# Optimization experiments

Measured on AMD Instinct MI355X. Metric: run time of the kernel, lower is better.

Reference implementation:

```python
import jax, jax.numpy as jnp
import numpy as np

B, T, C, N = 4, 12, 64, 10000
H = 64            # d_inner (GRU hidden)
L = 2             # num_layers
NE = 2000         # number of static hyperedges
NNZ = 80000       # incidence list length
TOPK = 10         # HGCNADP_topk
DE = 16           # HGCNADP_embed_dims
RATE = 0.5        # hyperedge_rate (blend static vs adaptive)


def setup_inputs() -> dict:
    key = jax.random.key(0)
    ks = jax.random.split(key, 10)
    scale = 0.05
    x = jax.random.normal(ks[0], (B, T, C, N), jnp.float32)
    node_idx = jax.random.randint(ks[1], (NNZ,), 0, N, jnp.int32)
    edge_idx = jax.random.randint(ks[2], (NNZ,), 0, NE, jnp.int32)
    hyperedge_index = jnp.stack([node_idx, edge_idx])  # (2, NNZ)
    node_embs = jax.random.normal(ks[3], (L, N, DE), jnp.float32) * 0.1
    W_zr = jax.random.normal(ks[4], (L, C + H, 2 * H), jnp.float32) * scale
    b_zr = jnp.zeros((L, 2 * H), jnp.float32)
    W_c = jax.random.normal(ks[5], (L, C + H, H), jnp.float32) * scale
    b_c = jnp.zeros((L, H), jnp.float32)
    W_out = jax.random.normal(ks[6], (L, H, C), jnp.float32) * scale
    b_out = jnp.zeros((L, C), jnp.float32)
    return {"x": x, "hyperedge_index": hyperedge_index, "node_embs": node_embs,
            "W_zr": W_zr, "b_zr": b_zr, "W_c": W_c, "b_c": b_c,
            "W_out": W_out, "b_out": b_out}


def reference(x, hyperedge_index, node_embs, W_zr, b_zr, W_c, b_c, W_out, b_out):
    # x: (B, T, C, N). Dropout is identity (eval mode).
    node_idx = hyperedge_index[0]
    edge_idx = hyperedge_index[1]
    edge_deg = jnp.zeros((NE,), x.dtype).at[edge_idx].add(1.0)
    inv_e = 1.0 / jnp.maximum(edge_deg, 1.0)
    node_deg = jnp.zeros((N,), x.dtype).at[node_idx].add(1.0)
    inv_n = 1.0 / jnp.maximum(node_deg, 1.0)

    def conv(f, topk_idx, topk_w):
        # f: (B, N, D). Static hypergraph pass: node -> hyperedge -> node.
        msg = jnp.take(f, node_idx, axis=1)                       # (B, NNZ, D)
        eagg = jnp.zeros((f.shape[0], NE, f.shape[2]), f.dtype).at[:, edge_idx].add(msg)
        eagg = eagg * inv_e[None, :, None]                        # (B, NE, D)
        stat = jnp.zeros_like(f).at[:, node_idx].add(jnp.take(eagg, edge_idx, axis=1))
        stat = stat * inv_n[None, :, None]                        # (B, N, D)
        # Adaptive top-k hyperedge aggregation (softmax-weighted neighbor sum).
        adp = jnp.einsum('bnkd,nk->bnd', jnp.take(f, topk_idx, axis=1), topk_w)
        return RATE * stat + (1.0 - RATE) * adp

    out = x
    for l in range(L):
        xl = out.transpose(0, 1, 3, 2)                            # (B, T, N, C)
        E = node_embs[l]
        scores = jax.nn.relu(E @ E.T)                             # (N, N)
        vals, idx = jax.lax.top_k(scores, TOPK)                   # (N, K)
        w = jax.nn.softmax(vals, axis=-1)
        Wz, bz = W_zr[l], b_zr[l]
        Wc_, bc_ = W_c[l], b_c[l]
        Wo, bo = W_out[l], b_out[l]

        def step(h, x_t):
            zr = jax.nn.sigmoid(conv(jnp.concatenate([x_t, h], -1), idx, w) @ Wz + bz)
            z, r = jnp.split(zr, 2, axis=-1)
            c = jnp.tanh(conv(jnp.concatenate([x_t, r * h], -1), idx, w) @ Wc_ + bc_)
            h_new = z * h + (1.0 - z) * c
            return h_new, h_new @ Wo + bo

        h0 = jnp.zeros((out.shape[0], N, H), x.dtype)
        _, ys = jax.lax.scan(step, h0, xl.transpose(1, 0, 2, 3))  # ys: (T, B, N, C)
        out = out + ys.transpose(1, 0, 3, 2)                      # residual, back to (B,T,C,N)
    return out
```

## Files before the change

kernel.cpp:

```cpp
#include <hip/hip_runtime.h>
#include <hip/hip_fp16.h>
#include <cstdio>

#define BB 4
#define TT 12
#define CC 64
#define NN 10000
#define HH 64
#define LL 2
#define NEDGE 2000
#define NNZT 80000
#define KTOP 10
#define DEMB 16
#define BT (BB*TT)
#define TOPK_BLKS 1250
#define TRN_BLKS 30048

typedef long long ll;
typedef unsigned long long u64;
typedef unsigned int u32;
typedef unsigned short ushort;

typedef short bf16x8 __attribute__((ext_vector_type(8)));
typedef float f32x4 __attribute__((ext_vector_type(4)));

__device__ __forceinline__ void up8(const uint4 v, float* f) {
  const __half2* p = reinterpret_cast<const __half2*>(&v);
  float2 t0 = __half22float2(p[0]);
  float2 t1 = __half22float2(p[1]);
  float2 t2 = __half22float2(p[2]);
  float2 t3 = __half22float2(p[3]);
  f[0]=t0.x; f[1]=t0.y; f[2]=t1.x; f[3]=t1.y;
  f[4]=t2.x; f[5]=t2.y; f[6]=t3.x; f[7]=t3.y;
}
__device__ __forceinline__ uint4 pk8(const float* f) {
  __half2 h0 = __floats2half2_rn(f[0], f[1]);
  __half2 h1 = __floats2half2_rn(f[2], f[3]);
  __half2 h2 = __floats2half2_rn(f[4], f[5]);
  __half2 h3 = __floats2half2_rn(f[6], f[7]);
  uint4 r;
  r.x = *reinterpret_cast<unsigned*>(&h0);
  r.y = *reinterpret_cast<unsigned*>(&h1);
  r.z = *reinterpret_cast<unsigned*>(&h2);
  r.w = *reinterpret_cast<unsigned*>(&h3);
  return r;
}
__device__ __forceinline__ ushort f2bf(float x) {
  u32 u = __float_as_uint(x);
  u32 r = u + 0x7FFFu + ((u >> 16) & 1u);
  return (ushort)(r >> 16);
}
__device__ __forceinline__ uint4 pk8bf(const float* f) {
  uint4 r;
  r.x = (u32)f2bf(f[0]) | ((u32)f2bf(f[1])<<16);
  r.y = (u32)f2bf(f[2]) | ((u32)f2bf(f[3])<<16);
  r.z = (u32)f2bf(f[4]) | ((u32)f2bf(f[5])<<16);
  r.w = (u32)f2bf(f[6]) | ((u32)f2bf(f[7])<<16);
  return r;
}

__global__ void deg_kernel(const int* __restrict__ nidx, const int* __restrict__ eidx,
                           int* __restrict__ ndeg, int* __restrict__ edeg) {
  int i = blockIdx.x*256 + threadIdx.x;
  if (i < NNZT) { atomicAdd(&ndeg[nidx[i]],1); atomicAdd(&edeg[eidx[i]],1); }
}

__global__ void exscan_kernel(const int* __restrict__ cnt, int* __restrict__ off, int n) {
  __shared__ int part[256];
  int tid = threadIdx.x;
  int chunk = (n + 255)/256;
  int lo = tid*chunk, hi = min(lo+chunk, n);
  int s = 0;
  for (int i=lo; i<hi; ++i) s += cnt[i];
  part[tid]=s; __syncthreads();
  if (tid==0){ int acc=0; for(int i=0;i<256;++i){int v=part[i];part[i]=acc;acc+=v;} off[n]=acc; }
  __syncthreads();
  int acc = part[tid];
  for (int i=lo; i<hi; ++i){ off[i]=acc; acc+=cnt[i]; }
}

__global__ void fill_csr_kernel(const int* __restrict__ nidx, const int* __restrict__ eidx,
                                const int* __restrict__ noff, const int* __restrict__ eoff,
                                int* __restrict__ ncur, int* __restrict__ ecur,
                                int* __restrict__ node_edges, int* __restrict__ edge_nodes) {
  int i = blockIdx.x*256 + threadIdx.x;
  if (i >= NNZT) return;
  int n = nidx[i], e = eidx[i];
  int pn = atomicAdd(&ncur[n],1);
  node_edges[noff[n]+pn] = e;
  int pe = atomicAdd(&ecur[e],1);
  edge_nodes[eoff[e]+pe] = n;
}

__global__ void invdeg_kernel(const int* __restrict__ ndeg, const int* __restrict__ edeg,
                              float* __restrict__ inv_n, float* __restrict__ inv_e) {
  int i = blockIdx.x*256+threadIdx.x;
  if (i < NN) inv_n[i] = 1.0f/fmaxf((float)ndeg[i],1.0f);
  if (i < NEDGE) inv_e[i] = 1.0f/fmaxf((float)edeg[i],1.0f);
}

__global__ void prep_w_kernel(const float* __restrict__ W_zr, const float* __restrict__ W_c,
                              const float* __restrict__ W_o,
                              short* __restrict__ Wz_swb, short* __restrict__ Wc_swb,
                              short* __restrict__ Wo_swb) {
  int l = blockIdx.y;
  const float* Wz = W_zr + (size_t)l*128*128;
  const float* Wc = W_c  + (size_t)l*128*64;
  const float* Wo = W_o  + (size_t)l*64*64;
  short* Wz_sw = Wz_swb + (size_t)l*16384;
  short* Wc_sw = Wc_swb + (size_t)l*8192;
  short* Wo_sw = Wo_swb + (size_t)l*4096;
  int idx = blockIdx.x*256 + threadIdx.x;
  if (idx < 16384) {
    int i = idx&7, lane = (idx>>3)&63, kk = (idx>>9)&3, tc = idx>>11;
    int k = kk*32 + (lane>>4)*8 + i, col = tc*16 + (lane&15);
    Wz_sw[idx] = (short)f2bf(Wz[k*128+col]);
  }
  if (idx < 8192) {
    int i = idx&7, lane = (idx>>3)&63, kk = (idx>>9)&3, tc = idx>>11;
    int k = kk*32 + (lane>>4)*8 + i, col = tc*16 + (lane&15);
    Wc_sw[idx] = (short)f2bf(Wc[k*64+col]);
  }
  if (idx < 4096) {
    int i = idx&7, lane = (idx>>3)&63, kk = (idx>>9)&1, tc = idx>>10;
    int k = kk*32 + (lane>>4)*8 + i, col = tc*16 + (lane&15);
    Wo_sw[idx] = (short)f2bf(Wo[k*64+col]);
  }
}

__device__ __forceinline__ u64 sortstep(u64 X, int j, bool dir, int lane) {
  u64 p = __shfl_xor(X, j);
  bool lower = ((lane & j) == 0);
  bool keep_min = (dir == lower);
  bool xlt = (X < p);
  u64 mn = xlt ? X : p;
  u64 mx = xlt ? p : X;
  return keep_min ? mn : mx;
}

__device__ __forceinline__ void reselect(u64* bq, u64& thr, int& cnt, int lane) {
  int tot = 10 + cnt;
  u64 A = (lane < tot)      ? bq[lane]      : 0ull;
  u64 B = (lane + 64 < tot) ? bq[lane + 64] : 0ull;
  for (int k = 2; k <= 32; k <<= 1) {
    for (int j = k >> 1; j >= 1; j >>= 1) {
      bool dir = ((lane & k) == 0);
      A = sortstep(A, j, dir, lane);
      B = sortstep(B, j, dir, lane);
    }
  }
  for (int j = 32; j >= 1; j >>= 1) {
    A = sortstep(A, j, true,  lane);
    B = sortstep(B, j, false, lane);
  }
  {
    bool lt = (A < B);
    u64 mn = lt ? A : B, mx = lt ? B : A;
    A = mn; B = mx;
  }
  for (int j = 32; j >= 1; j >>= 1) {
    A = sortstep(A, j, true, lane);
    B = sortstep(B, j, true, lane);
  }
  if (lane >= 54) bq[63 - lane] = B;
  thr = __shfl(B, 54);
  cnt = 0;
}

__device__ void topk_body(int layer, int qb, char* smem,
                          const float* __restrict__ embs, int2* __restrict__ tkc_b) {
  u64 (*buf)[128] = (u64(*)[128])smem;
  const float* E = embs + (ll)layer*NN*DEMB;
  int2* tkc = tkc_b + (ll)layer*NN*KTOP;
  int tid = threadIdx.x;
  int wv = tid >> 6, lane = tid & 63;
  int qbase = qb*16 + wv*4;
  const float4* E4 = (const float4*)E;
  float4 q[4][4];
  #pragma unroll
  for (int u=0;u<4;++u) {
    int n = qbase + u;
    #pragma unroll
    for (int j=0;j<4;++j) q[u][j] = E4[(ll)n*4 + j];
  }
  u64 thr[4] = {0,0,0,0};
  float thrf[4] = {0.f,0.f,0.f,0.f};
  int cnt[4] = {0,0,0,0};
  buf[tid>>4][tid&15] = 0ull;
  for (int cb=0; cb<NN; cb+=64) {
    int cand = cb + lane;
    bool valid = (cand < NN);
    int ca = valid ? cand : 0;
    float4 a0 = E4[(ll)ca*4], a1 = E4[(ll)ca*4+1], a2 = E4[(ll)ca*4+2], a3 = E4[(ll)ca*4+3];
    u64 low = (u64)(0x00FFFFFFu - (unsigned)cand);
    float sv[4];
    #pragma unroll
    for (int u=0;u<4;++u) {
      float dot = q[u][0].x*a0.x + q[u][0].y*a0.y + q[u][0].z*a0.z + q[u][0].w*a0.w
                + q[u][1].x*a1.x + q[u][1].y*a1.y + q[u][1].z*a1.z + q[u][1].w*a1.w
                + q[u][2].x*a2.x + q[u][2].y*a2.y + q[u][2].z*a2.z + q[u][2].w*a2.w
                + q[u][3].x*a3.x + q[u][3].y*a3.y + q[u][3].z*a3.z + q[u][3].w*a3.w;
      float s = fmaxf(dot, 0.f);
      sv[u] = valid ? s : -1.f;
    }
    #pragma unroll
    for (int u=0;u<4;++u) {
      u64 mask = __ballot(sv[u] >= thrf[u]);
      if (mask) {
        if (sv[u] >= thrf[u]) {
          u64 key = ((u64)__float_as_uint(sv[u]) << 32) | low;
          int myofs = (int)__popcll(mask & ((1ull<<lane)-1ull));
          buf[wv*4+u][10 + cnt[u] + myofs] = key;
        }
        cnt[u] += (int)__popcll(mask);
        if (cnt[u] >= 40) {
          reselect(&buf[wv*4+u][0], thr[u], cnt[u], lane);
          thrf[u] = __uint_as_float((u32)(thr[u] >> 32));
        }
      }
    }
  }
  #pragma unroll
  for (int u=0;u<4;++u) {
    u64* bq = &buf[wv*4+u][0];
    if (cnt[u] > 0) reselect(bq, thr[u], cnt[u], lane);
    u64 k10 = (lane < 10) ? bq[lane] : 0ull;
    float v = __uint_as_float((unsigned)(k10 >> 32));
    int idx = 0x00FFFFFF - (int)(k10 & 0xFFFFFFFFull);
    float v0 = __shfl(v, 0);
    float e = (lane < 10) ? expf(v - v0) : 0.f;
    float s = e;
    for (int o=1;o<16;o<<=1) s += __shfl_xor(s, o);
    if (lane < 10) {
      int n = qbase + u;
      tkc[n*KTOP + lane] = make_int2(idx, __float_as_int(e / s));
    }
  }
}

__device__ void transpose_body(int tb, char* smem,
                               const float* __restrict__ src, __half* __restrict__ dst) {
  float (*tile)[33] = (float(*)[33])smem;
  int tid = threadIdx.x;
  int tx = tid & 31, ty = tid >> 5;
  int bt = tb / 626;
  int rem = tb % 626;
  int n0 = (rem % 313)*32, c0 = (rem/313)*32;
  for (int i=ty; i<32; i+=8) {
    int c = c0+i, nn = n0+tx;
    tile[i][tx] = (nn<NN)? src[((ll)bt*CC + c)*NN + nn] : 0.0f;
  }
  __syncthreads();
  for (int i=ty; i<32; i+=8) {
    int nn = n0+i, c = c0+tx;
    if (nn<NN) dst[((ll)bt*NN+nn)*64 + c] = __float2half_rn(tile[tx][i]);
  }
}

__global__ void __launch_bounds__(256) mega1_kernel(const float* __restrict__ embs,
                                                    int2* __restrict__ tkc,
                                                    const float* __restrict__ x,
                                                    __half* __restrict__ xt) {
  __shared__ __align__(16) char smem[16384];
  int bid = blockIdx.x;
  if (bid < TOPK_BLKS) topk_body(bid/625, bid%625, smem, embs, tkc);
  else transpose_body(bid - TOPK_BLKS, smem, x, xt);
}

__global__ void transpose_kernel(const float* __restrict__ src, __half* __restrict__ dst) {
  __shared__ __align__(16) char smem[4352];
  int tb = (blockIdx.z*626) + blockIdx.y*313 + blockIdx.x;
  transpose_body(tb, smem, src, dst);
}

__global__ void __launch_bounds__(256) edge_agg_kernel(
    const uint4* __restrict__ f8, uint4* __restrict__ eagg8,
    const int* __restrict__ eoff, const int* __restrict__ enodes,
    const float* __restrict__ inv_e) {
  __shared__ int en_s[1088];
  __shared__ int jo_s[17];
  int tid = threadIdx.x;
  int e0 = blockIdx.x*16;
  int s = blockIdx.y;
  if (tid < 17) jo_s[tid] = eoff[e0 + tid];
  __syncthreads();
  int jb0 = jo_s[0], cnt = jo_s[16] - jb0;
  bool stg = (cnt <= 1088);
  if (stg) for (int i = tid; i < cnt; i += 256) en_s[i] = enodes[jb0 + i];
  __syncthreads();
  int esub = tid>>4;
  int e = e0 + esub;
  int hsel = (tid>>3)&1;
  int lane8 = tid&7;
  int j0 = jo_s[esub] - jb0, j1 = jo_s[esub+1] - jb0;
  const uint4* fb = f8 + (ll)s*NN*8;
  float acc[8] = {0,0,0,0,0,0,0,0};
  for (int j = j0 + hsel; j < j1; j += 2) {
    int node = stg ? en_s[j] : enodes[jb0+j];
    float t[8]; up8(fb[(ll)node*8 + lane8], t);
    #pragma unroll
    for (int q=0;q<8;++q) acc[q] += t[q];
  }
  #pragma unroll
  for (int q=0;q<8;++q) acc[q] += __shfl_xor(acc[q], 8);
  if (hsel == 0) {
    float sc = inv_e[e];
    #pragma unroll
    for (int q=0;q<8;++q) acc[q] *= sc;
    eagg8[((ll)s*NEDGE+e)*8 + lane8] = pk8(acc);
  }
}

__global__ void __launch_bounds__(256) conv_x_kernel(
    const uint4* __restrict__ xt8, const uint4* __restrict__ eagg8,
    const int* __restrict__ noff, const int* __restrict__ nedges,
    const float* __restrict__ inv_n,
    const int2* __restrict__ tkc,
    uint4* __restrict__ cx8) {
  __shared__ int tki_s[32][KTOP];
  __shared__ float tkw_s[32][KTOP];
  __shared__ int ne_s[640];
  __shared__ int no_s[33];
  int tid = threadIdx.x; int s = blockIdx.y; int n0 = blockIdx.x*32;
  if (tid < 33) no_s[tid] = noff[min(n0 + tid, NN)];
  for (int i=tid; i<32*KTOP; i+=256) {
    int r=i/KTOP, k=i%KTOP; int n = n0+r;
    int2 p = (n<NN)? tkc[n*KTOP+k] : make_int2(0,0);
    tki_s[r][k] = p.x;
    tkw_s[r][k] = __int_as_float(p.y);
  }
  __syncthreads();
  int jb0 = no_s[0], cnt = no_s[32] - jb0;
  bool stg = (cnt <= 640);
  if (stg) for (int i=tid; i<cnt; i+=256) ne_s[i] = nedges[jb0+i];
  __syncthreads();
  int row = tid>>3, lane8 = tid&7;
  int n = n0 + row;
  if (n >= NN) return;
  float stv[8] = {0,0,0,0,0,0,0,0};
  const uint4* eb = eagg8 + (ll)s*NEDGE*8;
  int j0 = no_s[row] - jb0, j1 = no_s[row+1] - jb0;
  for (int j=j0;j<j1;++j) {
    int eidx = stg ? ne_s[j] : nedges[jb0+j];
    float t[8]; up8(eb[(ll)eidx*8 + lane8], t);
    #pragma unroll
    for (int q=0;q<8;++q) stv[q] += t[q];
  }
  float sc = 0.5f*inv_n[n];
  float adv[8] = {0,0,0,0,0,0,0,0};
  const uint4* xb = xt8 + (ll)s*NN*8;
  #pragma unroll
  for (int k=0;k<KTOP;++k) {
    float w = tkw_s[row][k];
    float t[8]; up8(xb[(ll)tki_s[row][k]*8 + lane8], t);
    #pragma unroll
    for (int q=0;q<8;++q) adv[q] += w*t[q];
  }
  float r8[8];
  #pragma unroll
  for (int q=0;q<8;++q) r8[q] = sc*stv[q] + 0.5f*adv[q];
  cx8[((ll)s*NN+n)*8+lane8] = pk8bf(r8);
}

__global__ void __launch_bounds__(256) step0_kernel(
    const uint4* __restrict__ cx8,
    const short* __restrict__ Wz_sw, const float* __restrict__ bz,
    const short* __restrict__ Wc_sw, const float* __restrict__ bc,
    const short* __restrict__ Wo_sw, const float* __restrict__ bo,
    __half* __restrict__ h, float* __restrict__ out) {
  __shared__ __align__(16) short in_bf[32][72];
  __shared__ __align__(16) short hn[32][72];
  __shared__ __align__(16) float yt[64][36];
  int tid = threadIdx.x;
  int b = blockIdx.y; int n0 = blockIdx.x*32;
  int bt = b*TT;
  {
    int row = tid>>3, lane8 = tid&7;
    int n = n0 + row;
    uint4 cxv4 = make_uint4(0,0,0,0);
    if (n < NN) cxv4 = cx8[((ll)bt*NN + n)*8 + lane8];
    *(uint4*)&in_bf[row][lane8*8] = cxv4;
  }
  __syncthreads();
  int wv = tid>>6, lane = tid&63;
  int m = lane&15, g = lane>>4;
  #pragma unroll
  for (int q=0;q<2;++q) {
    int T = wv + 4*q;
    int tr = T>>2, tc = T&3;
    f32x4 az = {0.f,0.f,0.f,0.f};
    f32x4 ac = {0.f,0.f,0.f,0.f};
    #pragma unroll
    for (int kk=0;kk<2;++kk) {
      bf16x8 a = *(const bf16x8*)&in_bf[tr*16 + m][kk*32 + g*8];
      bf16x8 bwz = *(const bf16x8*)&Wz_sw[((tc*4+kk)*64 + lane)*8];
      bf16x8 bwc = *(const bf16x8*)&Wc_sw[((tc*4+kk)*64 + lane)*8];
      az = __builtin_amdgcn_mfma_f32_16x16x32_bf16(a, bwz, az, 0, 0, 0);
      ac = __builtin_amdgcn_mfma_f32_16x16x32_bf16(a, bwc, ac, 0, 0, 0);
    }
    int col = tc*16 + m;
    float bzv = bz[col], bcv = bc[col];
    #pragma unroll
    for (int r=0;r<4;++r) {
      int row = tr*16 + g*4 + r;
      int n = n0 + row;
      float z = 1.0f/(1.0f+expf(-(az[r]+bzv)));
      float cval = tanhf(ac[r]+bcv);
      float hnew = (1.0f-z)*cval;
      if (n < NN) h[((ll)b*NN+n)*64+col] = __float2half_rn(hnew);
      hn[row][col] = (short)f2bf(hnew);
    }
  }
  __syncthreads();
  #pragma unroll
  for (int q=0;q<2;++q) {
    int T = wv + 4*q;
    int tr = T>>2, tc = T&3;
    f32x4 acc = {0.f,0.f,0.f,0.f};
    #pragma unroll
    for (int kk=0;kk<2;++kk) {
      bf16x8 a = *(const bf16x8*)&hn[tr*16 + m][kk*32 + g*8];
      bf16x8 bw = *(const bf16x8*)&Wo_sw[((tc*2+kk)*64 + lane)*8];
      acc = __builtin_amdgcn_mfma_f32_16x16x32_bf16(a, bw, acc, 0, 0, 0);
    }
    int col = tc*16 + m;
    float bias = bo[col];
    #pragma unroll
    for (int r=0;r<4;++r) {
      int row = tr*16 + g*4 + r;
      yt[col][row] = acc[r] + bias;
    }
  }
  __syncthreads();
  #pragma unroll
  for (int kk=0;kk<2;++kk) {
    int slot = tid + kk*256;
    int col = slot>>3, q = slot&7;
    int n = n0 + q*4;
    if (n < NN) {
      float4 y = *(const float4*)&yt[col][q*4];
      float4* dst = (float4*)&out[((ll)bt*64+col)*NN + n];
      float4 cur = *dst;
      cur.x += y.x; cur.y += y.y; cur.z += y.z; cur.w += y.w;
      *dst = cur;
    }
  }
}

__global__ void __launch_bounds__(256) step_zr_kernel(
    const uint4* __restrict__ h8, const uint4* __restrict__ cx8,
    const uint4* __restrict__ eagg8,
    const short* __restrict__ Wz_sw, const float* __restrict__ bz,
    const int* __restrict__ noff, const int* __restrict__ nedges,
    const float* __restrict__ inv_n,
    const int2* __restrict__ tkc,
    const __half* __restrict__ hs,
    __half* __restrict__ rh, __half* __restrict__ zout, int t) {
  __shared__ __align__(16) short in_bf[32][136];
  __shared__ int tki_s[32][KTOP];
  __shared__ float tkw_s[32][KTOP];
  __shared__ int ne_s[640];
  __shared__ int no_s[33];
  int tid = threadIdx.x;
  int b = blockIdx.y; int n0 = blockIdx.x*32;
  int bt = b*TT + t;
  if (tid < 33) no_s[tid] = noff[min(n0 + tid, NN)];
  for (int i=tid; i<32*KTOP; i+=256) {
    int r=i/KTOP, k=i%KTOP; int n=n0+r;
    int2 p = (n<NN)? tkc[n*KTOP+k] : make_int2(0,0);
    tki_s[r][k] = p.x;
    tkw_s[r][k] = __int_as_float(p.y);
  }
  __syncthreads();
  int jb0 = no_s[0], ecnt = no_s[32] - jb0;
  bool stg = (ecnt <= 640);
  if (stg) for (int i=tid; i<ecnt; i+=256) ne_s[i] = nedges[jb0+i];
  __syncthreads();
  {
    int row = tid>>3, lane8 = tid&7;
    int n = n0 + row;
    uint4 cxv4 = make_uint4(0,0,0,0);
    float chv[8] = {0,0,0,0,0,0,0,0};
    if (n < NN) {
      cxv4 = cx8[((ll)bt*NN + n)*8 + lane8];
      float stv[8] = {0,0,0,0,0,0,0,0};
      int j0 = no_s[row] - jb0, j1 = no_s[row+1] - jb0;
      const uint4* eb = eagg8 + (ll)b*NEDGE*8;
      for (int j=j0;j<j1;++j) {
        int eidx = stg ? ne_s[j] : nedges[jb0+j];
        float t8[8]; up8(eb[(ll)eidx*8 + lane8], t8);
        #pragma unroll
        for (int q=0;q<8;++q) stv[q] += t8[q];
      }
      float sc = 0.5f*inv_n[n];
      const uint4* hb = h8 + (ll)b*NN*8;
      float adv[8] = {0,0,0,0,0,0,0,0};
      #pragma unroll
      for (int k=0;k<KTOP;++k) {
        float w = tkw_s[row][k];
        float t8[8]; up8(hb[(ll)tki_s[row][k]*8 + lane8], t8);
        #pragma unroll
        for (int q=0;q<8;++q) adv[q] += w*t8[q];
      }
      #pragma unroll
      for (int q=0;q<8;++q) chv[q] = sc*stv[q] + 0.5f*adv[q];
    }
    *(uint4*)&in_bf[row][lane8*8]    = cxv4;
    *(uint4*)&in_bf[row][64+lane8*8] = pk8bf(chv);
  }
  __syncthreads();
  int wv = tid>>6, lane = tid&63;
  int m = lane&15, g = lane>>4;
  #pragma unroll
  for (int q=0;q<4;++q) {
    int T = wv*4 + q;
    int tr = T>>3, tc = T&7;
    f32x4 acc = {0.f,0.f,0.f,0.f};
    #pragma unroll
    for (int kk=0;kk<4;++kk) {
      bf16x8 a = *(const bf16x8*)&in_bf[tr*16 + m][kk*32 + g*8];
      bf16x8 bf = *(const bf16x8*)&Wz_sw[((tc*4+kk)*64 + lane)*8];
      acc = __builtin_amdgcn_mfma_f32_16x16x32_bf16(a, bf, acc, 0, 0, 0);
    }
    int col = tc*16 + m;
    float bias = bz[col];
    #pragma unroll
    for (int r=0;r<4;++r) {
      int row = tr*16 + g*4 + r;
      int n = n0 + row;
      if (n < NN) {
        float v = 1.0f/(1.0f+expf(-(acc[r]+bias)));
        if (col < 64) zout[((ll)b*NN+n)*64+col] = __float2half_rn(v);
        else {
          int c = col-64;
          float hv = __half2float(hs[((ll)b*NN+n)*64+c]);
          rh[((ll)b*NN+n)*64+c] = __float2half_rn(v*hv);
        }
      }
    }
  }
}

__global__ void __launch_bounds__(256) step_hy_kernel(
    const uint4* __restrict__ rh8, const uint4* __restrict__ cx8,
    const uint4* __restrict__ eagg8,
    const short* __restrict__ Wc_sw, const float* __restrict__ bc,
    const short* __restrict__ Wo_sw, const float* __restrict__ bo,
    const int* __restrict__ noff, const int* __restrict__ nedges,
    const float* __restrict__ inv_n,
    const int2* __restrict__ tkc,
    const __half* __restrict__ zbuf, __half* __restrict__ h,
    float* __restrict__ out, int t) {
  __shared__ __align__(16) short in_bf[32][136];
  __shared__ __align__(16) short hn[32][72];
  __shared__ __align__(16) float yt[64][36];
  __shared__ int tki_s[32][KTOP];
  __shared__ float tkw_s[32][KTOP];
  __shared__ int ne_s[640];
  __shared__ int no_s[33];
  int tid = threadIdx.x;
  int b = blockIdx.y; int n0 = blockIdx.x*32;
  int bt = b*TT + t;
  if (tid < 33) no_s[tid] = noff[min(n0 + tid, NN)];
  for (int i=tid; i<32*KTOP; i+=256) {
    int r=i/KTOP, k=i%KTOP; int n=n0+r;
    int2 p = (n<NN)? tkc[n*KTOP+k] : make_int2(0,0);
    tki_s[r][k] = p.x;
    tkw_s[r][k] = __int_as_float(p.y);
  }
  __syncthreads();
  int jb0 = no_s[0], ecnt = no_s[32] - jb0;
  bool stg = (ecnt <= 640);
  if (stg) for (int i=tid; i<ecnt; i+=256) ne_s[i] = nedges[jb0+i];
  __syncthreads();
  {
    int row = tid>>3, lane8 = tid&7;
    int n = n0 + row;
    uint4 cxv4 = make_uint4(0,0,0,0);
    float chv[8] = {0,0,0,0,0,0,0,0};
    if (n < NN) {
      cxv4 = cx8[((ll)bt*NN + n)*8 + lane8];
      float stv[8] = {0,0,0,0,0,0,0,0};
      int j0 = no_s[row] - jb0, j1 = no_s[row+1] - jb0;
      const uint4* eb = eagg8 + (ll)b*NEDGE*8;
      for (int j=j0;j<j1;++j) {
        int eidx = stg ? ne_s[j] : nedges[jb0+j];
        float t8[8]; up8(eb[(ll)eidx*8 + lane8], t8);
        #pragma unroll
        for (int q=0;q<8;++q) stv[q] += t8[q];
      }
      float sc = 0.5f*inv_n[n];
      const uint4* rb = rh8 + (ll)b*NN*8;
      float adv[8] = {0,0,0,0,0,0,0,0};
      #pragma unroll
      for (int k=0;k<KTOP;++k) {
        float w = tkw_s[row][k];
        float t8[8]; up8(rb[(ll)tki_s[row][k]*8 + lane8], t8);
        #pragma unroll
        for (int q=0;q<8;++q) adv[q] += w*t8[q];
      }
      #pragma unroll
      for (int q=0;q<8;++q) chv[q] = sc*stv[q] + 0.5f*adv[q];
    }
    *(uint4*)&in_bf[row][lane8*8]    = cxv4;
    *(uint4*)&in_bf[row][64+lane8*8] = pk8bf(chv);
  }
  __syncthreads();
  int wv = tid>>6, lane = tid&63;
  int m = lane&15, g = lane>>4;
  #pragma unroll
  for (int q=0;q<2;++q) {
    int T = wv + 4*q;
    int tr = T>>2, tc = T&3;
    f32x4 acc = {0.f,0.f,0.f,0.f};
    #pragma unroll
    for (int kk=0;kk<4;++kk) {
      bf16x8 a = *(const bf16x8*)&in_bf[tr*16 + m][kk*32 + g*8];
      bf16x8 bf = *(const bf16x8*)&Wc_sw[((tc*4+kk)*64 + lane)*8];
      acc = __builtin_amdgcn_mfma_f32_16x16x32_bf16(a, bf, acc, 0, 0, 0);
    }
    int col = tc*16 + m;
    float bias = bc[col];
    #pragma unroll
    for (int r=0;r<4;++r) {
      int row = tr*16 + g*4 + r;
      int n = n0 + row;
      float hnew = 0.0f;
      if (n < NN) {
        float cval = tanhf(acc[r]+bias);
        float z = __half2float(zbuf[((ll)b*NN+n)*64+col]);
        float hv = __half2float(h[((ll)b*NN+n)*64+col]);
        hnew = z*hv + (1.0f-z)*cval;
        h[((ll)b*NN+n)*64+col] = __float2half_rn(hnew);
      }
      hn[row][col] = (short)f2bf(hnew);
    }
  }
  __syncthreads();
  #pragma unroll
  for (int q=0;q<2;++q) {
    int T = wv + 4*q;
    int tr = T>>2, tc = T&3;
    f32x4 acc = {0.f,0.f,0.f,0.f};
    #pragma unroll
    for (int kk=0;kk<2;++kk) {
      bf16x8 a = *(const bf16x8*)&hn[tr*16 + m][kk*32 + g*8];
      bf16x8 bf = *(const bf16x8*)&Wo_sw[((tc*2+kk)*64 + lane)*8];
      acc = __builtin_amdgcn_mfma_f32_16x16x32_bf16(a, bf, acc, 0, 0, 0);
    }
    int col = tc*16 + m;
    float bias = bo[col];
    #pragma unroll
    for (int r=0;r<4;++r) {
      int row = tr*16 + g*4 + r;
      yt[col][row] = acc[r] + bias;
    }
  }
  __syncthreads();
  #pragma unroll
  for (int kk=0;kk<2;++kk) {
    int slot = tid + kk*256;
    int col = slot>>3, q = slot&7;
    int n = n0 + q*4;
    if (n < NN) {
      float4 y = *(const float4*)&yt[col][q*4];
      float4* dst = (float4*)&out[((ll)bt*64+col)*NN + n];
      float4 cur = *dst;
      cur.x += y.x; cur.y += y.y; cur.z += y.z; cur.w += y.w;
      *dst = cur;
    }
  }
}

extern "C" void kernel_launch(void* const* d_in, const int* in_sizes, int n_in,
                              void* d_out, int out_size, void* d_ws, size_t ws_size,
                              hipStream_t stream) {
  const float* x    = (const float*)d_in[0];
  const int*  hidx  = (const int*)d_in[1];
  const float* embs = (const float*)d_in[2];
  const float* W_zr = (const float*)d_in[3];
  const float* b_zr = (const float*)d_in[4];
  const float* W_c  = (const float*)d_in[5];
  const float* b_c  = (const float*)d_in[6];
  const float* W_out= (const float*)d_in[7];
  const float* b_out= (const float*)d_in[8];
  const int* node_idx = hidx;
  const int* edge_idx = hidx + NNZT;

  char* ws = (char*)d_ws;
  size_t off = 0;
  auto alloc = [&](size_t bytes) -> void* {
    void* p = ws + off; off += (bytes + 255) & ~(size_t)255; return p;
  };
  __half* xt    = (__half*)alloc((size_t)BT*NN*64*2);
  __half* cx    = (__half*)alloc((size_t)BT*NN*64*2);
  __half* eaggx = (__half*)alloc((size_t)BT*NEDGE*64*2);
  __half* eaggh = (__half*)alloc((size_t)BB*NEDGE*64*2);
  __half* hbuf  = (__half*)alloc((size_t)BB*NN*64*2);
  __half* rhbuf = (__half*)alloc((size_t)BB*NN*64*2);
  __half* zbuf  = (__half*)alloc((size_t)BB*NN*64*2);
  short* Wz_sw = (short*)alloc((size_t)LL*16384*2);
  short* Wc_sw = (short*)alloc((size_t)LL*8192*2);
  short* Wo_sw = (short*)alloc((size_t)LL*4096*2);
  int2* tkc    = (int2*)alloc((size_t)LL*NN*KTOP*8);
  float* inv_e = (float*)alloc(NEDGE*4);
  float* inv_n = (float*)alloc(NN*4);
  int* ndeg    = (int*)alloc(NN*4);
  int* edeg    = (int*)alloc(NEDGE*4);
  int* noff    = (int*)alloc((NN+1)*4);
  int* eoff    = (int*)alloc((NEDGE+1)*4);
  int* ncur    = (int*)alloc(NN*4);
  int* ecur    = (int*)alloc(NEDGE*4);
  int* nedges  = (int*)alloc(NNZT*4);
  int* enodes  = (int*)alloc(NNZT*4);
  if (off > ws_size) {
    fprintf(stderr, "kernel_launch: ws too small, need %zu have %zu\n", off, ws_size);
    return;
  }

  hipMemcpyAsync(d_out, x, (size_t)BB*TT*CC*NN*4, hipMemcpyDeviceToDevice, stream);

  hipMemsetAsync(ndeg, 0, NN*4, stream);
  hipMemsetAsync(edeg, 0, NEDGE*4, stream);
  hipMemsetAsync(ncur, 0, NN*4, stream);
  hipMemsetAsync(ecur, 0, NEDGE*4, stream);
  deg_kernel<<<(NNZT+255)/256,256,0,stream>>>(node_idx, edge_idx, ndeg, edeg);
  exscan_kernel<<<1,256,0,stream>>>(ndeg, noff, NN);
  exscan_kernel<<<1,256,0,stream>>>(edeg, eoff, NEDGE);
  fill_csr_kernel<<<(NNZT+255)/256,256,0,stream>>>(node_idx, edge_idx, noff, eoff,
                                                   ncur, ecur, nedges, enodes);
  invdeg_kernel<<<(NN+255)/256,256,0,stream>>>(ndeg, edeg, inv_n, inv_e);

  prep_w_kernel<<<dim3(64,LL),256,0,stream>>>(W_zr, W_c, W_out, Wz_sw, Wc_sw, Wo_sw);
  float* outp = (float*)d_out;
  mega1_kernel<<<TOPK_BLKS + TRN_BLKS,256,0,stream>>>(embs, tkc, outp, xt);

  for (int l=0; l<LL; ++l) {
    const short* Wzs = Wz_sw + (size_t)l*16384;
    const short* Wcs = Wc_sw + (size_t)l*8192;
    const short* Wos = Wo_sw + (size_t)l*4096;
    const float* bz = b_zr + l*128;
    const float* bc = b_c + l*64;
    const float* bo = b_out + l*64;
    const int2* tkcl = tkc + (size_t)l*NN*KTOP;
    if (l > 0)
      transpose_kernel<<<dim3(313, 2, BT), 256, 0, stream>>>(outp, xt);
    edge_agg_kernel<<<dim3(125, BT),256,0,stream>>>(
        (const uint4*)xt, (uint4*)eaggx, eoff, enodes, inv_e);
    conv_x_kernel<<<dim3(313, BT),256,0,stream>>>(
        (const uint4*)xt, (const uint4*)eaggx, noff, nedges, inv_n, tkcl, (uint4*)cx);
    step0_kernel<<<dim3(313, BB),256,0,stream>>>(
        (const uint4*)cx, Wzs, bz, Wcs, bc, Wos, bo, hbuf, outp);
    for (int t=1; t<TT; ++t) {
      edge_agg_kernel<<<dim3(125, BB),256,0,stream>>>(
          (const uint4*)hbuf, (uint4*)eaggh, eoff, enodes, inv_e);
      step_zr_kernel<<<dim3(313, BB),256,0,stream>>>(
          (const uint4*)hbuf, (const uint4*)cx, (const uint4*)eaggh, Wzs, bz,
          noff, nedges, inv_n, tkcl, hbuf, rhbuf, zbuf, t);
      edge_agg_kernel<<<dim3(125, BB),256,0,stream>>>(
          (const uint4*)rhbuf, (uint4*)eaggh, eoff, enodes, inv_e);
      step_hy_kernel<<<dim3(313, BB),256,0,stream>>>(
          (const uint4*)rhbuf, (const uint4*)cx, (const uint4*)eaggh, Wcs, bc, Wos, bo,
          noff, nedges, inv_n, tkcl, zbuf, hbuf, outp, t);
    }
  }
}
```

Baseline: 2.354 ms.

## Fuse hyperedge aggregation into GRU step kernels via fixed-point atomics

Removes the separate edge_agg launches in the recurrent loop. Each step kernel now scatters its new h or r*h values into double-buffered int32 hyperedge accumulators using scaled fixed-point atomicAdd, and the next kernel reads those sums. Each kernel also zeroes the accumulator buffer it no longer needs. Separately, the top-k scan now prefetches the next candidate tile's embeddings one iteration ahead. The cost is heavy atomic traffic, int32 accumulators that are wider than the fp16 ones they replace, a fixed-point precision and overflow risk, and zeroing that depends on buffer rotation across layers.

```diff
diff --git a/kernel.cpp b/kernel.cpp
--- a/kernel.cpp
+++ b/kernel.cpp
@@ -15,6 +15,8 @@
 #define BT (BB*TT)
 #define TOPK_BLKS 1250
 #define TRN_BLKS 30048
+#define SCALE_F 67108864.0f
+#define INV_SCALE 1.4901161193847656e-8f
 
 typedef long long ll;
 typedef unsigned long long u64;
@@ -57,6 +59,14 @@
   r.z = (u32)f2bf(f[4]) | ((u32)f2bf(f[5])<<16);
   r.w = (u32)f2bf(f[6]) | ((u32)f2bf(f[7])<<16);
   return r;
+}
+
+__device__ __forceinline__ void zero_duty(int* buf, int b, int blk) {
+  const int total = NEDGE*64;
+  int base = blk*409;
+  int hi = min(base+409, total);
+  int* p = buf + (ll)b*total;
+  for (int i = base + threadIdx.x; i < hi; i += 256) p[i] = 0;
 }
 
 __global__ void deg_kernel(const int* __restrict__ nidx, const int* __restrict__ eidx,
@@ -187,11 +197,21 @@
   float thrf[4] = {0.f,0.f,0.f,0.f};
   int cnt[4] = {0,0,0,0};
   buf[tid>>4][tid&15] = 0ull;
+  float4 a0,a1,a2,a3;
+  {
+    int ca = (lane < NN) ? lane : 0;
+    a0=E4[(ll)ca*4]; a1=E4[(ll)ca*4+1]; a2=E4[(ll)ca*4+2]; a3=E4[(ll)ca*4+3];
+  }
   for (int cb=0; cb<NN; cb+=64) {
+    float4 b0,b1,b2,b3;
+    int ncb = cb + 64;
+    if (ncb < NN) {
+      int cand2 = ncb + lane;
+      int ca2 = (cand2 < NN) ? cand2 : 0;
+      b0=E4[(ll)ca2*4]; b1=E4[(ll)ca2*4+1]; b2=E4[(ll)ca2*4+2]; b3=E4[(ll)ca2*4+3];
+    }
     int cand = cb + lane;
     bool valid = (cand < NN);
-    int ca = valid ? cand : 0;
-    float4 a0 = E4[(ll)ca*4], a1 = E4[(ll)ca*4+1], a2 = E4[(ll)ca*4+2], a3 = E4[(ll)ca*4+3];
     u64 low = (u64)(0x00FFFFFFu - (unsigned)cand);
     float sv[4];
     #pragma unroll
@@ -219,6 +239,7 @@
         }
       }
     }
+    a0=b0; a1=b1; a2=b2; a3=b3;
   }
   #pragma unroll
   for (int u=0;u<4;++u) {
@@ -367,13 +388,25 @@
     const short* __restrict__ Wz_sw, const float* __restrict__ bz,
     const short* __restrict__ Wc_sw, const float* __restrict__ bc,
     const short* __restrict__ Wo_sw, const float* __restrict__ bo,
-    __half* __restrict__ h, float* __restrict__ out) {
+    const int* __restrict__ noff, const int* __restrict__ nedges,
+    const float* __restrict__ inv_e,
+    __half* __restrict__ h, float* __restrict__ out,
+    int* __restrict__ ieh_dst, int* __restrict__ zero1, int* __restrict__ zero2) {
   __shared__ __align__(16) short in_bf[32][72];
   __shared__ __align__(16) short hn[32][72];
   __shared__ __align__(16) float yt[64][36];
+  __shared__ int ne_s[640];
+  __shared__ int no_s[33];
   int tid = threadIdx.x;
   int b = blockIdx.y; int n0 = blockIdx.x*32;
   int bt = b*TT;
+  zero_duty(zero1, b, blockIdx.x);
+  zero_duty(zero2, b, blockIdx.x);
+  if (tid < 33) no_s[tid] = noff[min(n0 + tid, NN)];
+  __syncthreads();
+  int jb0 = no_s[0], ecnt = no_s[32] - jb0;
+  bool stg = (ecnt <= 640);
+  if (stg) for (int i=tid; i<ecnt; i+=256) ne_s[i] = nedges[jb0+i];
   {
     int row = tid>>3, lane8 = tid&7;
     int n = n0 + row;
@@ -407,7 +440,15 @@
       float z = 1.0f/(1.0f+expf(-(az[r]+bzv)));
       float cval = tanhf(ac[r]+bcv);
       float hnew = (1.0f-z)*cval;
-      if (n < NN) h[((ll)b*NN+n)*64+col] = __float2half_rn(hnew);
+      if (n < NN) {
+        h[((ll)b*NN+n)*64+col] = __float2half_rn(hnew);
+        int j0 = no_s[row]-jb0, j1 = no_s[row+1]-jb0;
+        for (int j=j0;j<j1;++j) {
+          int e = stg ? ne_s[j] : nedges[jb0+j];
+          atomicAdd(&ieh_dst[((ll)b*NEDGE+e)*64 + col],
+                    __float2int_rn(hnew*inv_e[e]*SCALE_F));
+        }
+      }
       hn[row][col] = (short)f2bf(hnew);
     }
   }
@@ -449,13 +490,14 @@
 
 __global__ void __launch_bounds__(256) step_zr_kernel(
     const uint4* __restrict__ h8, const uint4* __restrict__ cx8,
-    const uint4* __restrict__ eagg8,
+    const int* __restrict__ ieh_cur,
     const short* __restrict__ Wz_sw, const float* __restrict__ bz,
     const int* __restrict__ noff, const int* __restrict__ nedges,
-    const float* __restrict__ inv_n,
+    const float* __restrict__ inv_n, const float* __restrict__ inv_e,
     const int2* __restrict__ tkc,
     const __half* __restrict__ hs,
-    __half* __restrict__ rh, __half* __restrict__ zout, int t) {
+    __half* __restrict__ rh, __half* __restrict__ zout,
+    int* __restrict__ ierh_dst, int* __restrict__ ierh_zero, int t) {
   __shared__ __align__(16) short in_bf[32][136];
   __shared__ int tki_s[32][KTOP];
   __shared__ float tkw_s[32][KTOP];
@@ -464,6 +506,7 @@
   int tid = threadIdx.x;
   int b = blockIdx.y; int n0 = blockIdx.x*32;
   int bt = b*TT + t;
+  zero_duty(ierh_zero, b, blockIdx.x);
   if (tid < 33) no_s[tid] = noff[min(n0 + tid, NN)];
   for (int i=tid; i<32*KTOP; i+=256) {
     int r=i/KTOP, k=i%KTOP; int n=n0+r;
@@ -485,14 +528,15 @@
       cxv4 = cx8[((ll)bt*NN + n)*8 + lane8];
       float stv[8] = {0,0,0,0,0,0,0,0};
       int j0 = no_s[row] - jb0, j1 = no_s[row+1] - jb0;
-      const uint4* eb = eagg8 + (ll)b*NEDGE*8;
+      const int4* ebi = (const int4*)ieh_cur + (ll)b*NEDGE*16;
       for (int j=j0;j<j1;++j) {
         int eidx = stg ? ne_s[j] : nedges[jb0+j];
-        float t8[8]; up8(eb[(ll)eidx*8 + lane8], t8);
-        #pragma unroll
-        for (int q=0;q<8;++q) stv[q] += t8[q];
+        int4 v0 = ebi[(ll)eidx*16 + lane8*2];
+        int4 v1 = ebi[(ll)eidx*16 + lane8*2 + 1];
+        stv[0]+=(float)v0.x; stv[1]+=(float)v0.y; stv[2]+=(float)v0.z; stv[3]+=(float)v0.w;
+        stv[4]+=(float)v1.x; stv[5]+=(float)v1.y; stv[6]+=(float)v1.z; stv[7]+=(float)v1.w;
       }
-      float sc = 0.5f*inv_n[n];
+      float sc = 0.5f*inv_n[n]*INV_SCALE;
       const uint4* hb = h8 + (ll)b*NN*8;
       float adv[8] = {0,0,0,0,0,0,0,0};
       #pragma unroll
@@ -534,7 +578,14 @@
         else {
           int c = col-64;
           float hv = __half2float(hs[((ll)b*NN+n)*64+c]);
-          rh[((ll)b*NN+n)*64+c] = __float2half_rn(v*hv);
+          float rhv = v*hv;
+          rh[((ll)b*NN+n)*64+c] = __float2half_rn(rhv);
+          int j0 = no_s[row]-jb0, j1 = no_s[row+1]-jb0;
+          for (int j=j0;j<j1;++j) {
+            int e = stg ? ne_s[j] : nedges[jb0+j];
+            atomicAdd(&ierh_dst[((ll)b*NEDGE+e)*64 + c],
+                      __float2int_rn(rhv*inv_e[e]*SCALE_F));
+          }
         }
       }
     }
@@ -543,14 +594,15 @@
 
 __global__ void __launch_bounds__(256) step_hy_kernel(
     const uint4* __restrict__ rh8, const uint4* __restrict__ cx8,
-    const uint4* __restrict__ eagg8,
+    const int* __restrict__ ierh_cur,
     const short* __restrict__ Wc_sw, const float* __restrict__ bc,
     const short* __restrict__ Wo_sw, const float* __restrict__ bo,
     const int* __restrict__ noff, const int* __restrict__ nedges,
-    const float* __restrict__ inv_n,
+    const float* __restrict__ inv_n, const float* __restrict__ inv_e,
     const int2* __restrict__ tkc,
     const __half* __restrict__ zbuf, __half* __restrict__ h,
-    float* __restrict__ out, int t) {
+    float* __restrict__ out,
+    int* __restrict__ ieh_dst, int* __restrict__ ieh_zero, int t) {
   __shared__ __align__(16) short in_bf[32][136];
   __shared__ __align__(16) short hn[32][72];
   __shared__ __align__(16) float yt[64][36];
@@ -561,6 +613,7 @@
   int tid = threadIdx.x;
   int b = blockIdx.y; int n0 = blockIdx.x*32;
   int bt = b*TT + t;
+  zero_duty(ieh_zero, b, blockIdx.x);
   if (tid < 33) no_s[tid] = noff[min(n0 + tid, NN)];
   for (int i=tid; i<32*KTOP; i+=256) {
     int r=i/KTOP, k=i%KTOP; int n=n0+r;
@@ -582,14 +635,15 @@
       cxv4 = cx8[((ll)bt*NN + n)*8 + lane8];
       float stv[8] = {0,0,0,0,0,0,0,0};
       int j0 = no_s[row] - jb0, j1 = no_s[row+1] - jb0;
-      const uint4* eb = eagg8 + (ll)b*NEDGE*8;
+      const int4* ebi = (const int4*)ierh_cur + (ll)b*NEDGE*16;
       for (int j=j0;j<j1;++j) {
         int eidx = stg ? ne_s[j] : nedges[jb0+j];
-        float t8[8]; up8(eb[(ll)eidx*8 + lane8], t8);
-        #pragma unroll
-        for (int q=0;q<8;++q) stv[q] += t8[q];
+        int4 v0 = ebi[(ll)eidx*16 + lane8*2];
+        int4 v1 = ebi[(ll)eidx*16 + lane8*2 + 1];
+        stv[0]+=(float)v0.x; stv[1]+=(float)v0.y; stv[2]+=(float)v0.z; stv[3]+=(float)v0.w;
+        stv[4]+=(float)v1.x; stv[5]+=(float)v1.y; stv[6]+=(float)v1.z; stv[7]+=(float)v1.w;
       }
-      float sc = 0.5f*inv_n[n];
+      float sc = 0.5f*inv_n[n]*INV_SCALE;
       const uint4* rb = rh8 + (ll)b*NN*8;
       float adv[8] = {0,0,0,0,0,0,0,0};
       #pragma unroll
@@ -632,6 +686,12 @@
         float hv = __half2float(h[((ll)b*NN+n)*64+col]);
         hnew = z*hv + (1.0f-z)*cval;
         h[((ll)b*NN+n)*64+col] = __float2half_rn(hnew);
+        int j0 = no_s[row]-jb0, j1 = no_s[row+1]-jb0;
+        for (int j=j0;j<j1;++j) {
+          int e = stg ? ne_s[j] : nedges[jb0+j];
+          atomicAdd(&ieh_dst[((ll)b*NEDGE+e)*64 + col],
+                    __float2int_rn(hnew*inv_e[e]*SCALE_F));
+        }
       }
       hn[row][col] = (short)f2bf(hnew);
     }
@@ -695,10 +755,13 @@
   __half* xt    = (__half*)alloc((size_t)BT*NN*64*2);
   __half* cx    = (__half*)alloc((size_t)BT*NN*64*2);
   __half* eaggx = (__half*)alloc((size_t)BT*NEDGE*64*2);
-  __half* eaggh = (__half*)alloc((size_t)BB*NEDGE*64*2);
   __half* hbuf  = (__half*)alloc((size_t)BB*NN*64*2);
   __half* rhbuf = (__half*)alloc((size_t)BB*NN*64*2);
   __half* zbuf  = (__half*)alloc((size_t)BB*NN*64*2);
+  int* ieh0     = (int*)alloc((size_t)BB*NEDGE*64*4);
+  int* ieh1     = (int*)alloc((size_t)BB*NEDGE*64*4);
+  int* ierh0    = (int*)alloc((size_t)BB*NEDGE*64*4);
+  int* ierh1    = (int*)alloc((size_t)BB*NEDGE*64*4);
   short* Wz_sw = (short*)alloc((size_t)LL*16384*2);
   short* Wc_sw = (short*)alloc((size_t)LL*8192*2);
   short* Wo_sw = (short*)alloc((size_t)LL*4096*2);
@@ -717,6 +780,8 @@
     fprintf(stderr, "kernel_launch: ws too small, need %zu have %zu\n", off, ws_size);
     return;
   }
+  int* ieh[2]  = {ieh0, ieh1};
+  int* ierh[2] = {ierh0, ierh1};
 
   hipMemcpyAsync(d_out, x, (size_t)BB*TT*CC*NN*4, hipMemcpyDeviceToDevice, stream);
 
@@ -724,6 +789,10 @@
   hipMemsetAsync(edeg, 0, NEDGE*4, stream);
   hipMemsetAsync(ncur, 0, NN*4, stream);
   hipMemsetAsync(ecur, 0, NEDGE*4, stream);
+  hipMemsetAsync(ieh0, 0, (size_t)BB*NEDGE*64*4, stream);
+  hipMemsetAsync(ieh1, 0, (size_t)BB*NEDGE*64*4, stream);
+  hipMemsetAsync(ierh0, 0, (size_t)BB*NEDGE*64*4, stream);
+  hipMemsetAsync(ierh1, 0, (size_t)BB*NEDGE*64*4, stream);
   deg_kernel<<<(NNZT+255)/256,256,0,stream>>>(node_idx, edge_idx, ndeg, edeg);
   exscan_kernel<<<1,256,0,stream>>>(ndeg, noff, NN);
   exscan_kernel<<<1,256,0,stream>>>(edeg, eoff, NEDGE);
@@ -750,18 +819,18 @@
     conv_x_kernel<<<dim3(313, BT),256,0,stream>>>(
         (const uint4*)xt, (const uint4*)eaggx, noff, nedges, inv_n, tkcl, (uint4*)cx);
     step0_kernel<<<dim3(313, BB),256,0,stream>>>(
-        (const uint4*)cx, Wzs, bz, Wcs, bc, Wos, bo, hbuf, outp);
+        (const uint4*)cx, Wzs, bz, Wcs, bc, Wos, bo,
+        noff, nedges, inv_e, hbuf, outp, ieh[1], ieh[0], ierh[1]);
     for (int t=1; t<TT; ++t) {
-      edge_agg_kernel<<<dim3(125, BB),256,0,stream>>>(
-          (const uint4*)hbuf, (uint4*)eaggh, eoff, enodes, inv_e);
+      int pc = t & 1;
       step_zr_kernel<<<dim3(313, BB),256,0,stream>>>(
-          (const uint4*)hbuf, (const uint4*)cx, (const uint4*)eaggh, Wzs, bz,
-          noff, nedges, inv_n, tkcl, hbuf, rhbuf, zbuf, t);
-      edge_agg_kernel<<<dim3(125, BB),256,0,stream>>>(
-          (const uint4*)rhbuf, (uint4*)eaggh, eoff, enodes, inv_e);
+          (const uint4*)hbuf, (const uint4*)cx, ieh[pc], Wzs, bz,
+          noff, nedges, inv_n, inv_e, tkcl, hbuf, rhbuf, zbuf,
+          ierh[pc], ierh[1-pc], t);
       step_hy_kernel<<<dim3(313, BB),256,0,stream>>>(
-          (const uint4*)rhbuf, (const uint4*)cx, (const uint4*)eaggh, Wcs, bc, Wos, bo,
-          noff, nedges, inv_n, tkcl, zbuf, hbuf, outp, t);
-    }
-  }
-}
+          (const uint4*)rhbuf, (const uint4*)cx, ierh[pc], Wcs, bc, Wos, bo,
+          noff, nedges, inv_n, inv_e, tkcl, zbuf, hbuf, outp,
+          ieh[1-pc], ieh[pc], t);
+    }
+  }
+}
```

Result: slower. 6.050 ms (+157.0%).

## Screen top-k candidates with bf16 MFMA and rescore hits exactly in fp32

Applied to the files above, without the earlier changes.

Adds a kernel that converts the node embeddings to bf16 and rewrites the top-k scan so each wave computes a 16x16 score tile per step with an MFMA instruction. Candidates passing an approximate threshold (lowered by a small epsilon) are rescored in fp32 before insertion, and the selection buffer shrinks to a single 64-wide bitonic sort. The goal is to cut the fp32 dot-product work of the all-pairs top-k phase. The epsilon margin might miss true top-k entries if bf16 error exceeds it, and only 4 of the 16 MFMA rows are useful.

```diff
diff --git a/kernel.cpp b/kernel.cpp
--- a/kernel.cpp
+++ b/kernel.cpp
@@ -15,6 +15,7 @@
 #define BT (BB*TT)
 #define TOPK_BLKS 1250
 #define TRN_BLKS 30048
+#define EPS_TK 0.01f
 
 typedef long long ll;
 typedef unsigned long long u64;
@@ -128,6 +129,12 @@
   }
 }
 
+__global__ void ebf_kernel(const float* __restrict__ embs, ushort* __restrict__ Ebf) {
+  int l = blockIdx.y;
+  int i = blockIdx.x*256 + threadIdx.x;
+  if (i < NN*DEMB) Ebf[(ll)l*NN*DEMB + i] = f2bf(embs[(ll)l*NN*DEMB + i]);
+}
+
 __device__ __forceinline__ u64 sortstep(u64 X, int j, bool dir, int lane) {
   u64 p = __shfl_xor(X, j);
   bool lower = ((lane & j) == 0);
@@ -138,42 +145,31 @@
   return keep_min ? mn : mx;
 }
 
-__device__ __forceinline__ void reselect(u64* bq, u64& thr, int& cnt, int lane) {
+__device__ __forceinline__ void reselect64(u64* bq, u64& thr, int& cnt, int lane) {
   int tot = 10 + cnt;
-  u64 A = (lane < tot)      ? bq[lane]      : 0ull;
-  u64 B = (lane + 64 < tot) ? bq[lane + 64] : 0ull;
-  for (int k = 2; k <= 32; k <<= 1) {
+  u64 A = (lane < tot) ? bq[lane] : 0ull;
+  for (int k = 2; k <= 64; k <<= 1) {
     for (int j = k >> 1; j >= 1; j >>= 1) {
       bool dir = ((lane & k) == 0);
       A = sortstep(A, j, dir, lane);
-      B = sortstep(B, j, dir, lane);
-    }
-  }
-  for (int j = 32; j >= 1; j >>= 1) {
-    A = sortstep(A, j, true,  lane);
-    B = sortstep(B, j, false, lane);
-  }
-  {
-    bool lt = (A < B);
-    u64 mn = lt ? A : B, mx = lt ? B : A;
-    A = mn; B = mx;
-  }
-  for (int j = 32; j >= 1; j >>= 1) {
-    A = sortstep(A, j, true, lane);
-    B = sortstep(B, j, true, lane);
-  }
-  if (lane >= 54) bq[63 - lane] = B;
-  thr = __shfl(B, 54);
+    }
+  }
+  if (lane >= 54) bq[63 - lane] = A;
+  thr = __shfl(A, 54);
   cnt = 0;
 }
 
 __device__ void topk_body(int layer, int qb, char* smem,
-                          const float* __restrict__ embs, int2* __restrict__ tkc_b) {
-  u64 (*buf)[128] = (u64(*)[128])smem;
+                          const float* __restrict__ embs,
+                          const ushort* __restrict__ Ebf_all,
+                          int2* __restrict__ tkc_b) {
+  u64 (*buf)[64] = (u64(*)[64])smem;
   const float* E = embs + (ll)layer*NN*DEMB;
+  const ushort* Ebf = Ebf_all + (ll)layer*NN*DEMB;
   int2* tkc = tkc_b + (ll)layer*NN*KTOP;
   int tid = threadIdx.x;
   int wv = tid >> 6, lane = tid & 63;
+  int m = lane & 15, g = lane >> 4;
   int qbase = qb*16 + wv*4;
   const float4* E4 = (const float4*)E;
   float4 q[4][4];
@@ -183,47 +179,63 @@
     #pragma unroll
     for (int j=0;j<4;++j) q[u][j] = E4[(ll)n*4 + j];
   }
+  bf16x8 a_frag = {0,0,0,0,0,0,0,0};
+  if (m < 4 && g < 2)
+    a_frag = *(const bf16x8*)&Ebf[(ll)(qbase + m)*DEMB + g*8];
   u64 thr[4] = {0,0,0,0};
-  float thrf[4] = {0.f,0.f,0.f,0.f};
+  float tf[4] = {-1.0f,-1.0f,-1.0f,-1.0f};
   int cnt[4] = {0,0,0,0};
-  buf[tid>>4][tid&15] = 0ull;
-  for (int cb=0; cb<NN; cb+=64) {
-    int cand = cb + lane;
-    bool valid = (cand < NN);
-    int ca = valid ? cand : 0;
-    float4 a0 = E4[(ll)ca*4], a1 = E4[(ll)ca*4+1], a2 = E4[(ll)ca*4+2], a3 = E4[(ll)ca*4+3];
-    u64 low = (u64)(0x00FFFFFFu - (unsigned)cand);
-    float sv[4];
-    #pragma unroll
-    for (int u=0;u<4;++u) {
-      float dot = q[u][0].x*a0.x + q[u][0].y*a0.y + q[u][0].z*a0.z + q[u][0].w*a0.w
-                + q[u][1].x*a1.x + q[u][1].y*a1.y + q[u][1].z*a1.z + q[u][1].w*a1.w
-                + q[u][2].x*a2.x + q[u][2].y*a2.y + q[u][2].z*a2.z + q[u][2].w*a2.w
-                + q[u][3].x*a3.x + q[u][3].y*a3.y + q[u][3].z*a3.z + q[u][3].w*a3.w;
-      float s = fmaxf(dot, 0.f);
-      sv[u] = valid ? s : -1.f;
-    }
-    #pragma unroll
-    for (int u=0;u<4;++u) {
-      u64 mask = __ballot(sv[u] >= thrf[u]);
-      if (mask) {
-        if (sv[u] >= thrf[u]) {
-          u64 key = ((u64)__float_as_uint(sv[u]) << 32) | low;
-          int myofs = (int)__popcll(mask & ((1ull<<lane)-1ull));
-          buf[wv*4+u][10 + cnt[u] + myofs] = key;
-        }
-        cnt[u] += (int)__popcll(mask);
-        if (cnt[u] >= 40) {
-          reselect(&buf[wv*4+u][0], thr[u], cnt[u], lane);
-          thrf[u] = __uint_as_float((u32)(thr[u] >> 32));
+  for (int i=lane; i<256; i+=64) (&buf[wv*4][0])[i] = 0ull;
+  bf16x8 bcur = {0,0,0,0,0,0,0,0};
+  if (g < 2) bcur = *(const bf16x8*)&Ebf[(ll)m*DEMB + g*8];
+  for (int ct=0; ct<625; ++ct) {
+    bf16x8 bnxt = {0,0,0,0,0,0,0,0};
+    if (ct+1 < 625 && g < 2)
+      bnxt = *(const bf16x8*)&Ebf[(ll)((ct+1)*16 + m)*DEMB + g*8];
+    f32x4 acc = {0.f,0.f,0.f,0.f};
+    acc = __builtin_amdgcn_mfma_f32_16x16x32_bf16(a_frag, bcur, acc, 0, 0, 0);
+    float s0 = fmaxf(acc[0], 0.f), s1 = fmaxf(acc[1], 0.f);
+    float s2 = fmaxf(acc[2], 0.f), s3 = fmaxf(acc[3], 0.f);
+    bool h0 = (g==0) && (s0 >= tf[0]);
+    bool h1 = (g==0) && (s1 >= tf[1]);
+    bool h2 = (g==0) && (s2 >= tf[2]);
+    bool h3 = (g==0) && (s3 >= tf[3]);
+    u64 anym = __ballot(h0|h1|h2|h3);
+    if (anym) {
+      int cand0 = ct*16;
+      #pragma unroll
+      for (int r=0;r<4;++r) {
+        bool hr = (r==0)?h0:(r==1)?h1:(r==2)?h2:h3;
+        u64 mk = __ballot(hr);
+        if (mk) {
+          if (hr) {
+            int cand = cand0 + m;
+            float4 c0 = E4[(ll)cand*4],   c1 = E4[(ll)cand*4+1];
+            float4 c2 = E4[(ll)cand*4+2], c3 = E4[(ll)cand*4+3];
+            float dot = q[r][0].x*c0.x + q[r][0].y*c0.y + q[r][0].z*c0.z + q[r][0].w*c0.w
+                      + q[r][1].x*c1.x + q[r][1].y*c1.y + q[r][1].z*c1.z + q[r][1].w*c1.w
+                      + q[r][2].x*c2.x + q[r][2].y*c2.y + q[r][2].z*c2.z + q[r][2].w*c2.w
+                      + q[r][3].x*c3.x + q[r][3].y*c3.y + q[r][3].z*c3.z + q[r][3].w*c3.w;
+            float sx = fmaxf(dot, 0.f);
+            u64 key = ((u64)__float_as_uint(sx) << 32)
+                    | (u64)(0x00FFFFFFu - (unsigned)cand);
+            int ofs = (int)__popcll(mk & ((1ull<<lane)-1ull));
+            buf[wv*4+r][10 + cnt[r] + ofs] = key;
+          }
+          cnt[r] += (int)__popcll(mk);
+          if (cnt[r] >= 38) {
+            reselect64(&buf[wv*4+r][0], thr[r], cnt[r], lane);
+            tf[r] = __uint_as_float((u32)(thr[r] >> 32)) - EPS_TK;
+          }
         }
       }
     }
-  }
-  #pragma unroll
-  for (int u=0;u<4;++u) {
-    u64* bq = &buf[wv*4+u][0];
-    if (cnt[u] > 0) reselect(bq, thr[u], cnt[u], lane);
+    bcur = bnxt;
+  }
+  #pragma unroll
+  for (int r=0;r<4;++r) {
+    u64* bq = &buf[wv*4+r][0];
+    if (cnt[r] > 0) reselect64(bq, thr[r], cnt[r], lane);
     u64 k10 = (lane < 10) ? bq[lane] : 0ull;
     float v = __uint_as_float((unsigned)(k10 >> 32));
     int idx = 0x00FFFFFF - (int)(k10 & 0xFFFFFFFFull);
@@ -232,7 +244,7 @@
     float s = e;
     for (int o=1;o<16;o<<=1) s += __shfl_xor(s, o);
     if (lane < 10) {
-      int n = qbase + u;
+      int n = qbase + r;
       tkc[n*KTOP + lane] = make_int2(idx, __float_as_int(e / s));
     }
   }
@@ -258,12 +270,13 @@
 }
 
 __global__ void __launch_bounds__(256) mega1_kernel(const float* __restrict__ embs,
+                                                    const ushort* __restrict__ Ebf,
                                                     int2* __restrict__ tkc,
                                                     const float* __restrict__ x,
                                                     __half* __restrict__ xt) {
-  __shared__ __align__(16) char smem[16384];
+  __shared__ __align__(16) char smem[8192];
   int bid = blockIdx.x;
-  if (bid < TOPK_BLKS) topk_body(bid/625, bid%625, smem, embs, tkc);
+  if (bid < TOPK_BLKS) topk_body(bid/625, bid%625, smem, embs, Ebf, tkc);
   else transpose_body(bid - TOPK_BLKS, smem, x, xt);
 }
 
@@ -702,6 +715,7 @@
   short* Wz_sw = (short*)alloc((size_t)LL*16384*2);
   short* Wc_sw = (short*)alloc((size_t)LL*8192*2);
   short* Wo_sw = (short*)alloc((size_t)LL*4096*2);
+  ushort* Ebf  = (ushort*)alloc((size_t)LL*NN*DEMB*2);
   int2* tkc    = (int2*)alloc((size_t)LL*NN*KTOP*8);
   float* inv_e = (float*)alloc(NEDGE*4);
   float* inv_n = (float*)alloc(NN*4);
@@ -732,8 +746,9 @@
   invdeg_kernel<<<(NN+255)/256,256,0,stream>>>(ndeg, edeg, inv_n, inv_e);
 
   prep_w_kernel<<<dim3(64,LL),256,0,stream>>>(W_zr, W_c, W_out, Wz_sw, Wc_sw, Wo_sw);
+  ebf_kernel<<<dim3((NN*DEMB+255)/256, LL),256,0,stream>>>(embs, Ebf);
   float* outp = (float*)d_out;
-  mega1_kernel<<<TOPK_BLKS + TRN_BLKS,256,0,stream>>>(embs, tkc, outp, xt);
+  mega1_kernel<<<TOPK_BLKS + TRN_BLKS,256,0,stream>>>(embs, Ebf, tkc, outp, xt);
 
   for (int l=0; l<LL; ++l) {
     const short* Wzs = Wz_sw + (size_t)l*16384;
```

Result: slower. 2.811 ms (+19.4%).
